# Kernel tuning notes

Hardware: AMD Instinct MI355X
Metric: run time of the kernel (lower is better)

Reference implementation:

```python
import jax, jax.numpy as jnp
import numpy as np

B, L, H = 64, 512, 512          # batch, max_len, hidden_size (code requires H == L)
ITEM = 50001                    # item_num + 1
TEMP = 0.2                      # gumbel-sigmoid temperature
EPS = 1e-20


def setup_inputs() -> dict:
    key = jax.random.key(0)
    ks = jax.random.split(key, 16)
    lin = lambda k: jax.random.normal(k, (L, L), jnp.float32) * (1.0 / np.sqrt(L))
    U = jax.random.uniform(ks[13], (L, H), jnp.float32)
    gumbel = -jnp.log(-jnp.log(U + EPS) + EPS)
    return {
        "positives": jax.random.randint(ks[0], (B, L), 0, ITEM),
        "mask": jax.random.randint(ks[1], (B, L), 0, 2).astype(jnp.int32),
        "item_emb": jax.random.normal(ks[2], (ITEM, H), jnp.float32) * 0.02,
        "pos_emb": jax.random.normal(ks[3], (L, H), jnp.float32) * 0.02,
        "Wz": lin(ks[4]),
        "Wv": lin(ks[5]),
        "Wq": lin(ks[6]),
        "Wk": lin(ks[7]),
        "gamma_q": jax.random.normal(ks[8], (L,), jnp.float32) * 0.02,
        "beta_q": jnp.zeros((L,), jnp.float32),
        "gamma_k": jax.random.normal(ks[9], (L,), jnp.float32) * 0.02,
        "beta_k": jnp.zeros((L,), jnp.float32),
        "sparse_w": jax.random.uniform(ks[10], (L, H), jnp.float32, 0.2, 0.8),
        "gumbel": gumbel,
    }


def reference(positives, mask, item_emb, pos_emb, Wz, Wv, Wq, Wk,
              gamma_q, beta_q, gamma_k, beta_k, sparse_w, gumbel):
    # ---- merge_attn_masks: True = masked ----
    pad = ~(mask.astype(bool))[:, None, :]                 # [B,1,L]
    future = jnp.triu(jnp.ones((L, L), bool), k=1)         # strictly upper
    merged = pad | future[None]                            # [B,L,L]
    attn_mask = (~jnp.eye(L, dtype=bool))[None] & merged   # keep diagonal unmasked

    # ---- embeddings ----
    x = item_emb[positives] + pos_emb[None]                # [B,L,H]

    # ---- GAU-style projections (Linear acts on last dim, y = x @ W^T) ----
    z = jax.nn.silu(x @ Wz.T)                              # [B,L,H]
    v = jax.nn.silu(x @ Wv.T)                              # [B,L,H]
    q = (z @ Wq.T) * gamma_q + beta_q                      # OffsetScale head 0
    k = (z @ Wk.T) * gamma_k + beta_k

    # ---- relu^2 attention with bool mask added then zeroed ----
    m = attn_mask.astype(q.dtype)
    a = jnp.einsum('bld,bmd->blm', q, k) + m               # torch adds bool as 0/1
    a = a * (1.0 - m)                                      # a * ~attn_mask

    # ---- gumbel-sigmoid sparse mask (broadcast [L,L] over batch) ----
    smask = jax.nn.sigmoid((jnp.log(sparse_w / (1.0 - sparse_w)) + gumbel) / TEMP)
    a = smask[None] * a

    a = jnp.square(jax.nn.relu(a)) / (L * H)
    return a @ v                                           # [B,L,H]
```

## Files before the change

kernel.cpp:

```cpp
#include <hip/hip_runtime.h>
#include <hip/hip_fp16.h>
#include <math.h>

typedef _Float16 f16;
typedef unsigned int u32;
typedef _Float16 f16x8 __attribute__((ext_vector_type(8)));
typedef _Float16 f16x4 __attribute__((ext_vector_type(4)));
typedef float    f32x4 __attribute__((ext_vector_type(4)));

constexpr int LEN  = 512;
constexpr int HID  = 512;
constexpr int BATCH = 64;

__device__ __forceinline__ void gload16(const f16* g, f16* l) {
    __builtin_amdgcn_global_load_lds((const __attribute__((address_space(1))) u32*)g,
                                     (__attribute__((address_space(3))) u32*)l,
                                     16, 0, 0);
}

__device__ __forceinline__ float silu_f(float v) {
    return v * __builtin_amdgcn_rcpf(1.f + __expf(-v));
}

#define TUNIT 12288
#define EPIP  136

__device__ __forceinline__ void stage_pass(const f16* __restrict__ g, f16* l) {
    const int tid = threadIdx.x;
    const int row = tid >> 2;
    const int sc  = (tid & 3) ^ ((row >> 1) & 3);
    gload16(g + (size_t)row * 512 + sc * 8, l + (tid >> 6) * 512);
}

__device__ __forceinline__ void stage_tile(const f16* __restrict__ A,
                                           const f16* __restrict__ B,
                                           int kt, f16* buf) {
    stage_pass(A + kt * 32,             buf);
    stage_pass(A + kt * 32 + 128 * 512, buf + 4096);
    stage_pass(B + kt * 32,             buf + 8192);
}

__device__ __forceinline__ void gemm8b(const f16* __restrict__ A,
                                       const f16* __restrict__ B,
                                       int ksteps, f16* lds, f32x4 acc[4][4])
{
    const int lane = threadIdx.x & 63;
    const int wv   = threadIdx.x >> 6;
    const int wr = wv >> 1, wc = wv & 1;
    const int mf = lane & 15;
    const int slot = ((lane >> 4) ^ ((mf >> 1) & 3)) * 8;
    const int aoff = (wr * 64 + mf) * 32 + slot;
    const int boff = (wc * 64 + mf) * 32 + slot + 8192;

    #pragma unroll
    for (int m = 0; m < 4; ++m)
        #pragma unroll
        for (int n = 0; n < 4; ++n)
            acc[m][n] = (f32x4){0.f, 0.f, 0.f, 0.f};

    stage_tile(A, B, 0, lds);
    stage_tile(A, B, 1, lds + TUNIT);
    asm volatile("s_waitcnt vmcnt(3)" ::: "memory");
    __builtin_amdgcn_s_barrier();

    int cb = 0;
    for (int kt = 0; kt < ksteps; ++kt) {
        f16* buf = lds + cb * TUNIT;
        f16x8 af[4], bf[4];
        #pragma unroll
        for (int m = 0; m < 4; ++m) af[m] = *(const f16x8*)(buf + aoff + m * 512);
        #pragma unroll
        for (int n = 0; n < 4; ++n) bf[n] = *(const f16x8*)(buf + boff + n * 512);
        if (kt + 2 < ksteps) {
            int nb = cb + 2; if (nb >= 3) nb -= 3;
            stage_tile(A, B, kt + 2, lds + nb * TUNIT);
        }
        asm volatile("s_waitcnt lgkmcnt(0)" ::: "memory");
        __builtin_amdgcn_sched_barrier(0);
        __builtin_amdgcn_s_setprio(1);
        #pragma unroll
        for (int m = 0; m < 4; ++m)
            #pragma unroll
            for (int n = 0; n < 4; ++n)
                acc[m][n] = __builtin_amdgcn_mfma_f32_16x16x32_f16(af[m], bf[n], acc[m][n], 0, 0, 0);
        __builtin_amdgcn_s_setprio(0);
        if (kt + 3 <= ksteps) {
            asm volatile("s_waitcnt vmcnt(3)" ::: "memory");
            __builtin_amdgcn_s_barrier();
        } else if (kt + 2 == ksteps) {
            asm volatile("s_waitcnt vmcnt(0)" ::: "memory");
            __builtin_amdgcn_s_barrier();
        }
        cb = cb + 1; if (cb >= 3) cb = 0;
    }
}

#define EPI_IDX() \
    const int lane = threadIdx.x & 63, wv_ = threadIdx.x >> 6;  \
    const int wr = wv_ >> 1, wc = wv_ & 1;                      \
    const int c0 = lane & 15, r0 = (lane >> 4) * 4;

__device__ __forceinline__ void copy_half(const f16* lds, f16* __restrict__ gout,
                                          int ldo, int h) {
    const int tid = threadIdx.x;
    #pragma unroll
    for (int ph = 0; ph < 4; ++ph) {
        const int r = ph * 32 + (tid >> 4);
        const int c = (tid & 15) * 8;
        *(f16x8*)(gout + (size_t)(h * 128 + r) * ldo + c) = *(const f16x8*)(lds + r * EPIP + c);
    }
}

__global__ __launch_bounds__(512, 4) void k_zv8(const f16* __restrict__ x,
                                                const f16* __restrict__ Wzh,
                                                const f16* __restrict__ Wvh,
                                                f16* __restrict__ z,
                                                f16* __restrict__ vt)
{
    __shared__ __align__(16) f16 lds[3 * TUNIT];
    const int bid = blockIdx.x;
    const int s  = (bid & 7) + 8 * (bid >> 6);
    const int ci = (bid >> 3) & 7;
    const f16* A; const f16* Bm; f16* gout;
    if (ci < 4) {
        A = x + (size_t)s * 256 * HID;
        Bm = Wzh + (size_t)ci * 128 * HID;
        gout = z + (size_t)s * 256 * HID + ci * 128;
    } else {
        const int ht = (ci - 4) >> 1, lh = (ci - 4) & 1;
        A = Wvh + (size_t)ht * 256 * HID;
        Bm = x + ((size_t)s * 256 + lh * 128) * HID;
        gout = vt + (size_t)(s >> 1) * LEN * HID + (size_t)ht * 256 * LEN
                  + (s & 1) * 256 + lh * 128;
    }
    f32x4 acc[4][4];
    gemm8b(A, Bm, HID / 32, lds, acc);
    __syncthreads();
    EPI_IDX();
    #pragma unroll
    for (int h = 0; h < 2; ++h) {
        if ((wr >> 1) == h) {
            const int rb = (wr & 1) * 64;
            #pragma unroll
            for (int m = 0; m < 4; ++m)
                #pragma unroll
                for (int n = 0; n < 4; ++n)
                    #pragma unroll
                    for (int i = 0; i < 4; ++i)
                        lds[(rb + m * 16 + r0 + i) * EPIP + wc * 64 + n * 16 + c0] =
                            (f16)silu_f(acc[m][n][i]);
        }
        __syncthreads();
        copy_half(lds, gout, 512, h);
        __syncthreads();
    }
}

__global__ __launch_bounds__(512, 4) void k_qkp8(const f16* __restrict__ z,
                                                 const f16* __restrict__ Wqh,
                                                 const f16* __restrict__ Wkh,
                                                 const float* __restrict__ gq,
                                                 const float* __restrict__ bq,
                                                 const float* __restrict__ gk,
                                                 const float* __restrict__ bk,
                                                 f16* __restrict__ qh,
                                                 f16* __restrict__ kh)
{
    __shared__ __align__(16) f16 lds[3 * TUNIT];
    const int bid = blockIdx.x;
    const int s  = (bid & 7) + 8 * (bid >> 6);
    const int ci = (bid >> 3) & 7;
    const bool isq = ci < 4;
    const int nt = ci & 3;
    const f16* W = isq ? Wqh : Wkh;
    const float* g  = isq ? gq : gk;
    const float* be = isq ? bq : bk;
    f16* outp = isq ? qh : kh;
    f32x4 acc[4][4];
    gemm8b(z + (size_t)s * 256 * HID, W + (size_t)nt * 128 * HID, HID / 32, lds, acc);
    __syncthreads();
    EPI_IDX();
    f16* gbase = outp + (size_t)s * 256 * HID + nt * 128;
    #pragma unroll
    for (int h = 0; h < 2; ++h) {
        if ((wr >> 1) == h) {
            const int rb = (wr & 1) * 64;
            #pragma unroll
            for (int n = 0; n < 4; ++n) {
                const int col = wc * 64 + n * 16 + c0;
                const int jg = nt * 128 + col;
                const float ga = g[jg], ba = be[jg];
                #pragma unroll
                for (int m = 0; m < 4; ++m)
                    #pragma unroll
                    for (int i = 0; i < 4; ++i)
                        lds[(rb + m * 16 + r0 + i) * EPIP + col] =
                            (f16)((acc[m][n][i] * ga + ba) * 1024.f);
            }
        }
        __syncthreads();
        copy_half(lds, gbase, 512, h);
        __syncthreads();
    }
}

__constant__ int LT6[6] = {0,0,1,1,1,1};
__constant__ int MT6[6] = {0,1,0,1,2,3};

__global__ __launch_bounds__(512, 4) void k_qk8(const f16* __restrict__ q,
                                                const f16* __restrict__ kmat,
                                                const int* __restrict__ mask,
                                                const float* __restrict__ smask,
                                                f16* __restrict__ p)
{
    __shared__ __align__(16) f16 lds[3 * TUNIT];
    const int bid = blockIdx.x;
    const int t = (bid >> 3) % 6;
    const int b = (bid & 7) + 8 * (bid / 48);
    const int lt = LT6[t], mt = MT6[t];
    const size_t boff = (size_t)b * LEN * HID;
    f32x4 acc[4][4];
    gemm8b(q + boff + (size_t)lt * 256 * HID,
           kmat + boff + (size_t)mt * 128 * HID, HID / 32, lds, acc);
    __syncthreads();
    EPI_IDX();
    f16* gbase = p + (size_t)b * LEN * LEN + (size_t)lt * 256 * LEN + mt * 128;
    #pragma unroll
    for (int h = 0; h < 2; ++h) {
        if ((wr >> 1) == h) {
            const int rb = (wr & 1) * 64;
            #pragma unroll
            for (int n = 0; n < 4; ++n) {
                const int col = wc * 64 + n * 16 + c0;
                const int m_g = mt * 128 + col;
                const int keepcol = mask[b * LEN + m_g];
                #pragma unroll
                for (int m = 0; m < 4; ++m)
                    #pragma unroll
                    for (int i = 0; i < 4; ++i) {
                        const int row = rb + m * 16 + r0 + i;
                        const int l_g = lt * 256 + h * 128 + row;
                        const bool keep = (l_g == m_g) || ((m_g <= l_g) && (keepcol != 0));
                        float v = keep ? acc[m][n][i] * smask[l_g * LEN + m_g] : 0.f;
                        v = fmaxf(v, 0.f);
                        lds[row * EPIP + col] = (f16)(v * v);
                    }
            }
        }
        __syncthreads();
        copy_half(lds, gbase, 512, h);
        __syncthreads();
    }
}

__global__ __launch_bounds__(512, 4) void k_pv8(const f16* __restrict__ p,
                                                const f16* __restrict__ vt,
                                                float* __restrict__ out)
{
    __shared__ __align__(16) f16 lds[3 * TUNIT];
    const int bid = blockIdx.x;
    const int inner = (bid >> 3) & 7;
    const int b = (bid & 7) + 8 * (bid >> 6);
    const int lt = 1 - (inner >> 2), ht = inner & 3;
    f32x4 acc[4][4];
    gemm8b(p + (size_t)b * LEN * LEN + (size_t)lt * 256 * LEN,
           vt + (size_t)b * HID * LEN + (size_t)ht * 128 * LEN,
           (lt + 1) * 8, lds, acc);
    EPI_IDX();
    const float SCALE = 3.4694469519536142e-18f;
    #pragma unroll
    for (int m = 0; m < 4; ++m)
        #pragma unroll
        for (int n = 0; n < 4; ++n) {
            const int h = ht * 128 + wc * 64 + n * 16 + c0;
            #pragma unroll
            for (int i = 0; i < 4; ++i) {
                const int l = lt * 256 + wr * 64 + m * 16 + r0 + i;
                out[(size_t)b * LEN * HID + (size_t)l * HID + h] = acc[m][n][i] * SCALE;
            }
        }
}

__global__ __launch_bounds__(256) void k_prep(const int* __restrict__ pos,
                                              const float* __restrict__ item_emb,
                                              const float* __restrict__ pos_emb,
                                              f16* __restrict__ x,
                                              const float* __restrict__ Wz,
                                              const float* __restrict__ Wv,
                                              const float* __restrict__ Wq,
                                              const float* __restrict__ Wk,
                                              f16* __restrict__ Wzh,
                                              f16* __restrict__ Wvh,
                                              f16* __restrict__ Wqh,
                                              f16* __restrict__ Wkh,
                                              const float* __restrict__ sw,
                                              const float* __restrict__ gum,
                                              float* __restrict__ smask)
{
    const int bid = blockIdx.x;
    const int tid = threadIdx.x;
    if (bid < 16384) {
        const int t = bid * 256 + tid;
        const int i = t >> 7;
        const int c = t & 127;
        const int l = i & (LEN - 1);
        const int item = pos[i];
        const float4 a  = ((const float4*)(item_emb + (size_t)item * HID))[c];
        const float4 b4 = ((const float4*)(pos_emb + (size_t)l * HID))[c];
        f16x4 o = { (f16)(a.x + b4.x), (f16)(a.y + b4.y),
                    (f16)(a.z + b4.z), (f16)(a.w + b4.w) };
        *(f16x4*)(x + (size_t)t * 4) = o;
    } else if (bid < 16384 + 1024) {
        const int r = bid - 16384;
        const int w = r >> 8;
        const float* s = (w == 0) ? Wz : (w == 1) ? Wv : (w == 2) ? Wq : Wk;
        f16* d = (w == 0) ? Wzh : (w == 1) ? Wvh : (w == 2) ? Wqh : Wkh;
        const int t = (r & 255) * 256 + tid;
        const float4 v = ((const float4*)s)[t];
        f16x4 o = { (f16)v.x, (f16)v.y, (f16)v.z, (f16)v.w };
        *(f16x4*)(d + (size_t)t * 4) = o;
    } else {
        const int t = (bid - 16384 - 1024) * 256 + tid;
        const float4 w4 = ((const float4*)sw)[t];
        const float4 g4 = ((const float4*)gum)[t];
        float4 o;
        o.x = __builtin_amdgcn_rcpf(1.f + __expf(-(__logf(w4.x / (1.f - w4.x)) + g4.x) * 5.f));
        o.y = __builtin_amdgcn_rcpf(1.f + __expf(-(__logf(w4.y / (1.f - w4.y)) + g4.y) * 5.f));
        o.z = __builtin_amdgcn_rcpf(1.f + __expf(-(__logf(w4.z / (1.f - w4.z)) + g4.z) * 5.f));
        o.w = __builtin_amdgcn_rcpf(1.f + __expf(-(__logf(w4.w / (1.f - w4.w)) + g4.w) * 5.f));
        ((float4*)smask)[t] = o;
    }
}

extern "C" void kernel_launch(void* const* d_in, const int* in_sizes, int n_in,
                              void* d_out, int out_size, void* d_ws, size_t ws_size,
                              hipStream_t stream)
{
    const int*   positives = (const int*)  d_in[0];
    const int*   mask      = (const int*)  d_in[1];
    const float* item_emb  = (const float*)d_in[2];
    const float* pos_emb   = (const float*)d_in[3];
    const float* Wz        = (const float*)d_in[4];
    const float* Wv        = (const float*)d_in[5];
    const float* Wq        = (const float*)d_in[6];
    const float* Wk        = (const float*)d_in[7];
    const float* gamma_q   = (const float*)d_in[8];
    const float* beta_q    = (const float*)d_in[9];
    const float* gamma_k   = (const float*)d_in[10];
    const float* beta_k    = (const float*)d_in[11];
    const float* sparse_w  = (const float*)d_in[12];
    const float* gumbel    = (const float*)d_in[13];
    float* out = (float*)d_out;

    char* ws = (char*)d_ws;
    const size_t BUFB = (size_t)BATCH * LEN * HID * sizeof(f16);
    f16* buf0 = (f16*)ws;
    f16* buf1 = (f16*)(ws + BUFB);
    f16* buf2 = (f16*)(ws + 2 * BUFB);
    f16* Wzh  = (f16*)(ws + 3 * BUFB);
    f16* Wvh  = Wzh + LEN * HID;
    f16* Wqh  = Wvh + LEN * HID;
    f16* Wkh  = Wqh + LEN * HID;
    float* smask = (float*)(Wkh + LEN * HID);
    f16* qh = (f16*)d_out;
    f16* kh = qh + (size_t)BATCH * LEN * HID;

    k_prep<<<16384 + 1024 + 256, 256, 0, stream>>>(
        positives, item_emb, pos_emb, buf0,
        Wz, Wv, Wq, Wk, Wzh, Wvh, Wqh, Wkh,
        sparse_w, gumbel, smask);

    k_zv8<<<1024, 512, 0, stream>>>(buf0, Wzh, Wvh, buf1, buf2);

    k_qkp8<<<1024, 512, 0, stream>>>(buf1, Wqh, Wkh,
                                     gamma_q, beta_q, gamma_k, beta_k, qh, kh);

    k_qk8<<<384, 512, 0, stream>>>(qh, kh, mask, smask, buf0);

    k_pv8<<<512, 512, 0, stream>>>(buf0, buf2, out);
}
```

Before: 344.1 us.

## Fuse QK score and PV kernels into single attention kernel

Replaces the separate QK-score kernel, which wrote masked relu^2 scores to a global buffer, and the PV GEMM kernel with one kernel. For each key tile it computes scores, applies the mask and sparse mask in registers, stages the f16 scores in LDS, and multiplies by V, accumulating the output without a global round trip. The cost is that each output tile recomputes the QK products for its row panel, once per hidden slice (4x redundant QK work). It also reads V fragments straight from global memory instead of staging them, and uses more LDS, cutting occupancy to 2 blocks. Q and K move from the output buffer into separate workspace buffers.

Result: slower. 672.8 us (+95.5%).

```diff
diff --git a/kernel.cpp b/kernel.cpp
--- a/kernel.cpp
+++ b/kernel.cpp
@@ -24,6 +24,7 @@
 
 #define TUNIT 12288
 #define EPIP  136
+#define SBUF  36864
 
 __device__ __forceinline__ void stage_pass(const f16* __restrict__ g, f16* l) {
     const int tid = threadIdx.x;
@@ -204,79 +205,92 @@
     }
 }
 
-__constant__ int LT6[6] = {0,0,1,1,1,1};
-__constant__ int MT6[6] = {0,1,0,1,2,3};
-
-__global__ __launch_bounds__(512, 4) void k_qk8(const f16* __restrict__ q,
-                                                const f16* __restrict__ kmat,
-                                                const int* __restrict__ mask,
-                                                const float* __restrict__ smask,
-                                                f16* __restrict__ p)
-{
-    __shared__ __align__(16) f16 lds[3 * TUNIT];
-    const int bid = blockIdx.x;
-    const int t = (bid >> 3) % 6;
-    const int b = (bid & 7) + 8 * (bid / 48);
-    const int lt = LT6[t], mt = MT6[t];
-    const size_t boff = (size_t)b * LEN * HID;
-    f32x4 acc[4][4];
-    gemm8b(q + boff + (size_t)lt * 256 * HID,
-           kmat + boff + (size_t)mt * 128 * HID, HID / 32, lds, acc);
-    __syncthreads();
-    EPI_IDX();
-    f16* gbase = p + (size_t)b * LEN * LEN + (size_t)lt * 256 * LEN + mt * 128;
-    #pragma unroll
-    for (int h = 0; h < 2; ++h) {
-        if ((wr >> 1) == h) {
-            const int rb = (wr & 1) * 64;
-            #pragma unroll
-            for (int n = 0; n < 4; ++n) {
-                const int col = wc * 64 + n * 16 + c0;
-                const int m_g = mt * 128 + col;
-                const int keepcol = mask[b * LEN + m_g];
-                #pragma unroll
-                for (int m = 0; m < 4; ++m)
-                    #pragma unroll
-                    for (int i = 0; i < 4; ++i) {
-                        const int row = rb + m * 16 + r0 + i;
-                        const int l_g = lt * 256 + h * 128 + row;
-                        const bool keep = (l_g == m_g) || ((m_g <= l_g) && (keepcol != 0));
-                        float v = keep ? acc[m][n][i] * smask[l_g * LEN + m_g] : 0.f;
-                        v = fmaxf(v, 0.f);
-                        lds[row * EPIP + col] = (f16)(v * v);
-                    }
-            }
-        }
-        __syncthreads();
-        copy_half(lds, gbase, 512, h);
-        __syncthreads();
-    }
-}
-
-__global__ __launch_bounds__(512, 4) void k_pv8(const f16* __restrict__ p,
-                                                const f16* __restrict__ vt,
-                                                float* __restrict__ out)
-{
-    __shared__ __align__(16) f16 lds[3 * TUNIT];
+__global__ __launch_bounds__(512, 2) void k_attn(const f16* __restrict__ q,
+                                                 const f16* __restrict__ kmat,
+                                                 const f16* __restrict__ vt,
+                                                 const int* __restrict__ mask,
+                                                 const float* __restrict__ smask,
+                                                 float* __restrict__ out)
+{
+    __shared__ __align__(16) f16 lds[SBUF + 32768];
     const int bid = blockIdx.x;
     const int inner = (bid >> 3) & 7;
     const int b = (bid & 7) + 8 * (bid >> 6);
-    const int lt = 1 - (inner >> 2), ht = inner & 3;
-    f32x4 acc[4][4];
-    gemm8b(p + (size_t)b * LEN * LEN + (size_t)lt * 256 * LEN,
-           vt + (size_t)b * HID * LEN + (size_t)ht * 128 * LEN,
-           (lt + 1) * 8, lds, acc);
-    EPI_IDX();
+    const int lt = 1 - (inner >> 2), hh = inner & 3;
+    const int nmt = (lt + 1) * 2;
+
+    const int lane = threadIdx.x & 63;
+    const int wv   = threadIdx.x >> 6;
+    const int wr = wv >> 1, wc = wv & 1;
+    const int c0 = lane & 15, r0 = (lane >> 4) * 4;
+    const int mf = lane & 15;
+    const int kfr = (lane >> 4) * 8;
+    const int slot = ((lane >> 4) ^ ((mf >> 1) & 3)) * 8;
+
+    const size_t boff = (size_t)b * LEN * HID;
+    const f16* qpan = q + boff + (size_t)lt * 256 * HID;
+    const f16* vrow = vt + (size_t)b * HID * LEN + (size_t)(hh * 128 + wc * 64 + mf) * LEN;
+
+    f32x4 acc_o[4][4];
+    #pragma unroll
+    for (int m = 0; m < 4; ++m)
+        #pragma unroll
+        for (int n = 0; n < 4; ++n)
+            acc_o[m][n] = (f32x4){0.f, 0.f, 0.f, 0.f};
+
+    for (int mt = 0; mt < nmt; ++mt) {
+        f32x4 acc_s[4][4];
+        gemm8b(qpan, kmat + boff + (size_t)mt * 128 * HID, HID / 32, lds, acc_s);
+
+        #pragma unroll
+        for (int n = 0; n < 4; ++n) {
+            const int c_l = wc * 64 + n * 16 + c0;
+            const int m_g = mt * 128 + c_l;
+            const int keepcol = mask[b * LEN + m_g];
+            const int sb = c_l >> 5;
+            const int col5 = c_l & 31;
+            #pragma unroll
+            for (int m = 0; m < 4; ++m)
+                #pragma unroll
+                for (int i = 0; i < 4; ++i) {
+                    const int r_l = wr * 64 + m * 16 + r0 + i;
+                    const int l_g = lt * 256 + r_l;
+                    const bool keep = (l_g == m_g) || ((m_g <= l_g) && (keepcol != 0));
+                    float v = keep ? acc_s[m][n][i] * smask[l_g * LEN + m_g] : 0.f;
+                    v = fmaxf(v, 0.f);
+                    const int sch = (col5 >> 3) ^ ((r_l >> 1) & 3);
+                    lds[SBUF + sb * 8192 + r_l * 32 + sch * 8 + (col5 & 7)] = (f16)(v * v);
+                }
+        }
+        __syncthreads();
+
+        #pragma unroll
+        for (int ks = 0; ks < 4; ++ks) {
+            f16x8 af[4], bf[4];
+            #pragma unroll
+            for (int m = 0; m < 4; ++m)
+                af[m] = *(const f16x8*)(lds + SBUF + ks * 8192 + (wr * 64 + mf) * 32 + slot + m * 512);
+            #pragma unroll
+            for (int n = 0; n < 4; ++n)
+                bf[n] = *(const f16x8*)(vrow + (size_t)n * 16 * LEN + mt * 128 + ks * 32 + kfr);
+            #pragma unroll
+            for (int m = 0; m < 4; ++m)
+                #pragma unroll
+                for (int n = 0; n < 4; ++n)
+                    acc_o[m][n] = __builtin_amdgcn_mfma_f32_16x16x32_f16(af[m], bf[n], acc_o[m][n], 0, 0, 0);
+        }
+    }
+
     const float SCALE = 3.4694469519536142e-18f;
     #pragma unroll
     for (int m = 0; m < 4; ++m)
         #pragma unroll
         for (int n = 0; n < 4; ++n) {
-            const int h = ht * 128 + wc * 64 + n * 16 + c0;
+            const int h_g = hh * 128 + wc * 64 + n * 16 + c0;
             #pragma unroll
             for (int i = 0; i < 4; ++i) {
-                const int l = lt * 256 + wr * 64 + m * 16 + r0 + i;
-                out[(size_t)b * LEN * HID + (size_t)l * HID + h] = acc[m][n][i] * SCALE;
+                const int l_g = lt * 256 + wr * 64 + m * 16 + r0 + i;
+                out[(size_t)b * LEN * HID + (size_t)l_g * HID + h_g] = acc_o[m][n][i] * SCALE;
             }
         }
 }
@@ -357,13 +371,13 @@
     f16* buf0 = (f16*)ws;
     f16* buf1 = (f16*)(ws + BUFB);
     f16* buf2 = (f16*)(ws + 2 * BUFB);
-    f16* Wzh  = (f16*)(ws + 3 * BUFB);
+    f16* qh   = (f16*)(ws + 3 * BUFB);
+    f16* kh   = (f16*)(ws + 4 * BUFB);
+    f16* Wzh  = (f16*)(ws + 5 * BUFB);
     f16* Wvh  = Wzh + LEN * HID;
     f16* Wqh  = Wvh + LEN * HID;
     f16* Wkh  = Wqh + LEN * HID;
     float* smask = (float*)(Wkh + LEN * HID);
-    f16* qh = (f16*)d_out;
-    f16* kh = qh + (size_t)BATCH * LEN * HID;
 
     k_prep<<<16384 + 1024 + 256, 256, 0, stream>>>(
         positives, item_emb, pos_emb, buf0,
@@ -375,7 +389,5 @@
     k_qkp8<<<1024, 512, 0, stream>>>(buf1, Wqh, Wkh,
                                      gamma_q, beta_q, gamma_k, beta_k, qh, kh);
 
-    k_qk8<<<384, 512, 0, stream>>>(qh, kh, mask, smask, buf0);
-
-    k_pv8<<<512, 512, 0, stream>>>(buf0, buf2, out);
-}
+    k_attn<<<512, 512, 0, stream>>>(qh, kh, buf2, mask, smask, out);
+}
```

## Enlarge GEMM tiles to 256x256 with four-stage split-staged LDS pipeline

Applied to the files above, without the earlier changes.

Every GEMM kernel now computes a 256x256 output tile per block instead of 256x128. Each wave holds an 8x4 accumulator array, and each k-step is split into two MFMA halves, with the A and B loads for three steps ahead staged between them. This raises arithmetic intensity and reuse of staged LDS data and halves the grid sizes. The cost is more LDS (four 32KB stages) and more registers, so occupancy drops to 2 blocks per CU. The small grids, especially 192 blocks for QK^T, may underfill the GPU's CUs. q/k buffers also move from the output buffer to the workspace.

Measured after the change: 392.2 us. 14.0% more time.

```diff
diff --git a/kernel.cpp b/kernel.cpp
--- a/kernel.cpp
+++ b/kernel.cpp
@@ -22,8 +22,8 @@
     return v * __builtin_amdgcn_rcpf(1.f + __expf(-v));
 }
 
-#define TUNIT 12288
-#define EPIP  136
+#define TP 16384
+#define EP 264
 
 __device__ __forceinline__ void stage_pass(const f16* __restrict__ g, f16* l) {
     const int tid = threadIdx.x;
@@ -34,47 +34,52 @@
 
 __device__ __forceinline__ void stage_tile(const f16* __restrict__ A,
                                            const f16* __restrict__ B,
-                                           int kt, f16* buf) {
-    stage_pass(A + kt * 32,             buf);
-    stage_pass(A + kt * 32 + 128 * 512, buf + 4096);
-    stage_pass(B + kt * 32,             buf + 8192);
-}
-
-__device__ __forceinline__ void gemm8b(const f16* __restrict__ A,
+                                           int t, f16* buf) {
+    stage_pass(A + t * 32,             buf);
+    stage_pass(A + t * 32 + 128 * 512, buf + 4096);
+    stage_pass(B + t * 32,             buf + 8192);
+    stage_pass(B + t * 32 + 128 * 512, buf + 12288);
+}
+
+__device__ __forceinline__ void gemm8p(const f16* __restrict__ A,
                                        const f16* __restrict__ B,
-                                       int ksteps, f16* lds, f32x4 acc[4][4])
+                                       int nt, f16* lds, f32x4 acc[8][4])
 {
     const int lane = threadIdx.x & 63;
     const int wv   = threadIdx.x >> 6;
-    const int wr = wv >> 1, wc = wv & 1;
+    const int wr = wv >> 2, wc = wv & 3;
     const int mf = lane & 15;
     const int slot = ((lane >> 4) ^ ((mf >> 1) & 3)) * 8;
-    const int aoff = (wr * 64 + mf) * 32 + slot;
-    const int boff = (wc * 64 + mf) * 32 + slot + 8192;
-
-    #pragma unroll
-    for (int m = 0; m < 4; ++m)
+    const int abase = wr * 4096 + mf * 32 + slot;
+    const int bbase = 8192 + (wc >> 1) * 4096 + ((wc & 1) * 64 + mf) * 32 + slot;
+
+    #pragma unroll
+    for (int m = 0; m < 8; ++m)
         #pragma unroll
         for (int n = 0; n < 4; ++n)
             acc[m][n] = (f32x4){0.f, 0.f, 0.f, 0.f};
 
     stage_tile(A, B, 0, lds);
-    stage_tile(A, B, 1, lds + TUNIT);
-    asm volatile("s_waitcnt vmcnt(3)" ::: "memory");
+    stage_tile(A, B, 1, lds + TP);
+    stage_tile(A, B, 2, lds + 2 * TP);
+    asm volatile("s_waitcnt vmcnt(8)" ::: "memory");
     __builtin_amdgcn_s_barrier();
 
-    int cb = 0;
-    for (int kt = 0; kt < ksteps; ++kt) {
-        f16* buf = lds + cb * TUNIT;
+    for (int t = 0; t < nt; ++t) {
+        f16* buf  = lds + (t & 3) * TP;
+        f16* nbuf = lds + ((t + 3) & 3) * TP;
+        const bool st = (t + 3 < nt);
         f16x8 af[4], bf[4];
-        #pragma unroll
-        for (int m = 0; m < 4; ++m) af[m] = *(const f16x8*)(buf + aoff + m * 512);
-        #pragma unroll
-        for (int n = 0; n < 4; ++n) bf[n] = *(const f16x8*)(buf + boff + n * 512);
-        if (kt + 2 < ksteps) {
-            int nb = cb + 2; if (nb >= 3) nb -= 3;
-            stage_tile(A, B, kt + 2, lds + nb * TUNIT);
-        }
+
+        #pragma unroll
+        for (int m = 0; m < 4; ++m) af[m] = *(const f16x8*)(buf + abase + m * 512);
+        #pragma unroll
+        for (int n = 0; n < 4; ++n) bf[n] = *(const f16x8*)(buf + bbase + n * 512);
+        if (st) {
+            stage_pass(A + (t + 3) * 32,             nbuf);
+            stage_pass(A + (t + 3) * 32 + 128 * 512, nbuf + 4096);
+        }
+        __builtin_amdgcn_s_barrier();
         asm volatile("s_waitcnt lgkmcnt(0)" ::: "memory");
         __builtin_amdgcn_sched_barrier(0);
         __builtin_amdgcn_s_setprio(1);
@@ -84,70 +89,82 @@
             for (int n = 0; n < 4; ++n)
                 acc[m][n] = __builtin_amdgcn_mfma_f32_16x16x32_f16(af[m], bf[n], acc[m][n], 0, 0, 0);
         __builtin_amdgcn_s_setprio(0);
-        if (kt + 3 <= ksteps) {
-            asm volatile("s_waitcnt vmcnt(3)" ::: "memory");
-            __builtin_amdgcn_s_barrier();
-        } else if (kt + 2 == ksteps) {
-            asm volatile("s_waitcnt vmcnt(0)" ::: "memory");
-            __builtin_amdgcn_s_barrier();
-        }
-        cb = cb + 1; if (cb >= 3) cb = 0;
+        __builtin_amdgcn_s_barrier();
+
+        #pragma unroll
+        for (int m = 0; m < 4; ++m) af[m] = *(const f16x8*)(buf + abase + (m + 4) * 512);
+        if (st) {
+            stage_pass(B + (t + 3) * 32,             nbuf + 8192);
+            stage_pass(B + (t + 3) * 32 + 128 * 512, nbuf + 12288);
+        }
+        __builtin_amdgcn_s_barrier();
+        asm volatile("s_waitcnt lgkmcnt(0)" ::: "memory");
+        __builtin_amdgcn_sched_barrier(0);
+        __builtin_amdgcn_s_setprio(1);
+        #pragma unroll
+        for (int m = 0; m < 4; ++m)
+            #pragma unroll
+            for (int n = 0; n < 4; ++n)
+                acc[m + 4][n] = __builtin_amdgcn_mfma_f32_16x16x32_f16(af[m], bf[n], acc[m + 4][n], 0, 0, 0);
+        __builtin_amdgcn_s_setprio(0);
+        if (t < nt - 3)       { asm volatile("s_waitcnt vmcnt(8)" ::: "memory"); }
+        else if (t == nt - 3) { asm volatile("s_waitcnt vmcnt(4)" ::: "memory"); }
+        else if (t == nt - 2) { asm volatile("s_waitcnt vmcnt(0)" ::: "memory"); }
+        __builtin_amdgcn_s_barrier();
     }
 }
 
 #define EPI_IDX() \
     const int lane = threadIdx.x & 63, wv_ = threadIdx.x >> 6;  \
-    const int wr = wv_ >> 1, wc = wv_ & 1;                      \
+    const int wr = wv_ >> 2, wc = wv_ & 3;                      \
     const int c0 = lane & 15, r0 = (lane >> 4) * 4;
 
 __device__ __forceinline__ void copy_half(const f16* lds, f16* __restrict__ gout,
                                           int ldo, int h) {
     const int tid = threadIdx.x;
     #pragma unroll
-    for (int ph = 0; ph < 4; ++ph) {
-        const int r = ph * 32 + (tid >> 4);
-        const int c = (tid & 15) * 8;
-        *(f16x8*)(gout + (size_t)(h * 128 + r) * ldo + c) = *(const f16x8*)(lds + r * EPIP + c);
-    }
-}
-
-__global__ __launch_bounds__(512, 4) void k_zv8(const f16* __restrict__ x,
+    for (int ph = 0; ph < 8; ++ph) {
+        const int r = ph * 16 + (tid >> 5);
+        const int c = (tid & 31) * 8;
+        *(f16x8*)(gout + (size_t)(h * 128 + r) * ldo + c) = *(const f16x8*)(lds + r * EP + c);
+    }
+}
+
+__global__ __launch_bounds__(512, 2) void k_zv8(const f16* __restrict__ x,
                                                 const f16* __restrict__ Wzh,
                                                 const f16* __restrict__ Wvh,
                                                 f16* __restrict__ z,
                                                 f16* __restrict__ vt)
 {
-    __shared__ __align__(16) f16 lds[3 * TUNIT];
-    const int bid = blockIdx.x;
-    const int s  = (bid & 7) + 8 * (bid >> 6);
-    const int ci = (bid >> 3) & 7;
+    __shared__ __align__(16) f16 lds[4 * TP];
+    const int bid = blockIdx.x;
+    const int s  = (bid & 7) + 8 * (bid >> 5);
+    const int ci = (bid >> 3) & 3;
     const f16* A; const f16* Bm; f16* gout;
-    if (ci < 4) {
+    if (ci < 2) {
         A = x + (size_t)s * 256 * HID;
-        Bm = Wzh + (size_t)ci * 128 * HID;
-        gout = z + (size_t)s * 256 * HID + ci * 128;
+        Bm = Wzh + (size_t)ci * 256 * HID;
+        gout = z + (size_t)s * 256 * HID + ci * 256;
     } else {
-        const int ht = (ci - 4) >> 1, lh = (ci - 4) & 1;
+        const int ht = ci - 2;
         A = Wvh + (size_t)ht * 256 * HID;
-        Bm = x + ((size_t)s * 256 + lh * 128) * HID;
-        gout = vt + (size_t)(s >> 1) * LEN * HID + (size_t)ht * 256 * LEN
-                  + (s & 1) * 256 + lh * 128;
-    }
-    f32x4 acc[4][4];
-    gemm8b(A, Bm, HID / 32, lds, acc);
+        Bm = x + (size_t)s * 256 * HID;
+        gout = vt + (size_t)(s >> 1) * LEN * HID + (size_t)ht * 256 * LEN + (s & 1) * 256;
+    }
+    f32x4 acc[8][4];
+    gemm8p(A, Bm, 16, lds, acc);
+    EPI_IDX();
     __syncthreads();
-    EPI_IDX();
     #pragma unroll
     for (int h = 0; h < 2; ++h) {
-        if ((wr >> 1) == h) {
-            const int rb = (wr & 1) * 64;
-            #pragma unroll
-            for (int m = 0; m < 4; ++m)
+        if (wr == h) {
+            #pragma unroll
+            for (int m = 0; m < 8; ++m)
                 #pragma unroll
                 for (int n = 0; n < 4; ++n)
                     #pragma unroll
                     for (int i = 0; i < 4; ++i)
-                        lds[(rb + m * 16 + r0 + i) * EPIP + wc * 64 + n * 16 + c0] =
+                        lds[(m * 16 + r0 + i) * EP + wc * 64 + n * 16 + c0] =
                             (f16)silu_f(acc[m][n][i]);
         }
         __syncthreads();
@@ -156,7 +173,7 @@
     }
 }
 
-__global__ __launch_bounds__(512, 4) void k_qkp8(const f16* __restrict__ z,
+__global__ __launch_bounds__(512, 2) void k_qkp8(const f16* __restrict__ z,
                                                  const f16* __restrict__ Wqh,
                                                  const f16* __restrict__ Wkh,
                                                  const float* __restrict__ gq,
@@ -166,35 +183,34 @@
                                                  f16* __restrict__ qh,
                                                  f16* __restrict__ kh)
 {
-    __shared__ __align__(16) f16 lds[3 * TUNIT];
-    const int bid = blockIdx.x;
-    const int s  = (bid & 7) + 8 * (bid >> 6);
-    const int ci = (bid >> 3) & 7;
-    const bool isq = ci < 4;
-    const int nt = ci & 3;
+    __shared__ __align__(16) f16 lds[4 * TP];
+    const int bid = blockIdx.x;
+    const int s  = (bid & 7) + 8 * (bid >> 5);
+    const int ci = (bid >> 3) & 3;
+    const bool isq = ci < 2;
+    const int ct = ci & 1;
     const f16* W = isq ? Wqh : Wkh;
     const float* g  = isq ? gq : gk;
     const float* be = isq ? bq : bk;
     f16* outp = isq ? qh : kh;
-    f32x4 acc[4][4];
-    gemm8b(z + (size_t)s * 256 * HID, W + (size_t)nt * 128 * HID, HID / 32, lds, acc);
+    f32x4 acc[8][4];
+    gemm8p(z + (size_t)s * 256 * HID, W + (size_t)ct * 256 * HID, 16, lds, acc);
+    EPI_IDX();
+    f16* gbase = outp + (size_t)s * 256 * HID + ct * 256;
     __syncthreads();
-    EPI_IDX();
-    f16* gbase = outp + (size_t)s * 256 * HID + nt * 128;
     #pragma unroll
     for (int h = 0; h < 2; ++h) {
-        if ((wr >> 1) == h) {
-            const int rb = (wr & 1) * 64;
+        if (wr == h) {
             #pragma unroll
             for (int n = 0; n < 4; ++n) {
                 const int col = wc * 64 + n * 16 + c0;
-                const int jg = nt * 128 + col;
+                const int jg = ct * 256 + col;
                 const float ga = g[jg], ba = be[jg];
                 #pragma unroll
-                for (int m = 0; m < 4; ++m)
+                for (int m = 0; m < 8; ++m)
                     #pragma unroll
                     for (int i = 0; i < 4; ++i)
-                        lds[(rb + m * 16 + r0 + i) * EPIP + col] =
+                        lds[(m * 16 + r0 + i) * EP + col] =
                             (f16)((acc[m][n][i] * ga + ba) * 1024.f);
             }
         }
@@ -204,46 +220,45 @@
     }
 }
 
-__constant__ int LT6[6] = {0,0,1,1,1,1};
-__constant__ int MT6[6] = {0,1,0,1,2,3};
-
-__global__ __launch_bounds__(512, 4) void k_qk8(const f16* __restrict__ q,
+__constant__ int LT3[3] = {0, 1, 1};
+__constant__ int MT3[3] = {0, 0, 1};
+
+__global__ __launch_bounds__(512, 2) void k_qk8(const f16* __restrict__ q,
                                                 const f16* __restrict__ kmat,
                                                 const int* __restrict__ mask,
                                                 const float* __restrict__ smask,
                                                 f16* __restrict__ p)
 {
-    __shared__ __align__(16) f16 lds[3 * TUNIT];
-    const int bid = blockIdx.x;
-    const int t = (bid >> 3) % 6;
-    const int b = (bid & 7) + 8 * (bid / 48);
-    const int lt = LT6[t], mt = MT6[t];
+    __shared__ __align__(16) f16 lds[4 * TP];
+    const int bid = blockIdx.x;
+    const int tt = (bid >> 3) % 3;
+    const int b = (bid & 7) + 8 * (bid / 24);
+    const int lt = LT3[tt], mt = MT3[tt];
     const size_t boff = (size_t)b * LEN * HID;
-    f32x4 acc[4][4];
-    gemm8b(q + boff + (size_t)lt * 256 * HID,
-           kmat + boff + (size_t)mt * 128 * HID, HID / 32, lds, acc);
+    f32x4 acc[8][4];
+    gemm8p(q + boff + (size_t)lt * 256 * HID,
+           kmat + boff + (size_t)mt * 256 * HID, 16, lds, acc);
+    EPI_IDX();
+    f16* gbase = p + (size_t)b * LEN * LEN + (size_t)lt * 256 * LEN + mt * 256;
     __syncthreads();
-    EPI_IDX();
-    f16* gbase = p + (size_t)b * LEN * LEN + (size_t)lt * 256 * LEN + mt * 128;
     #pragma unroll
     for (int h = 0; h < 2; ++h) {
-        if ((wr >> 1) == h) {
-            const int rb = (wr & 1) * 64;
+        if (wr == h) {
             #pragma unroll
             for (int n = 0; n < 4; ++n) {
                 const int col = wc * 64 + n * 16 + c0;
-                const int m_g = mt * 128 + col;
+                const int m_g = mt * 256 + col;
                 const int keepcol = mask[b * LEN + m_g];
                 #pragma unroll
-                for (int m = 0; m < 4; ++m)
+                for (int m = 0; m < 8; ++m)
                     #pragma unroll
                     for (int i = 0; i < 4; ++i) {
-                        const int row = rb + m * 16 + r0 + i;
+                        const int row = m * 16 + r0 + i;
                         const int l_g = lt * 256 + h * 128 + row;
                         const bool keep = (l_g == m_g) || ((m_g <= l_g) && (keepcol != 0));
                         float v = keep ? acc[m][n][i] * smask[l_g * LEN + m_g] : 0.f;
                         v = fmaxf(v, 0.f);
-                        lds[row * EPIP + col] = (f16)(v * v);
+                        lds[row * EP + col] = (f16)(v * v);
                     }
             }
         }
@@ -253,30 +268,30 @@
     }
 }
 
-__global__ __launch_bounds__(512, 4) void k_pv8(const f16* __restrict__ p,
+__global__ __launch_bounds__(512, 2) void k_pv8(const f16* __restrict__ p,
                                                 const f16* __restrict__ vt,
                                                 float* __restrict__ out)
 {
-    __shared__ __align__(16) f16 lds[3 * TUNIT];
-    const int bid = blockIdx.x;
-    const int inner = (bid >> 3) & 7;
-    const int b = (bid & 7) + 8 * (bid >> 6);
-    const int lt = 1 - (inner >> 2), ht = inner & 3;
-    f32x4 acc[4][4];
-    gemm8b(p + (size_t)b * LEN * LEN + (size_t)lt * 256 * LEN,
-           vt + (size_t)b * HID * LEN + (size_t)ht * 128 * LEN,
+    __shared__ __align__(16) f16 lds[4 * TP];
+    const int bid = blockIdx.x;
+    const int inner = (bid >> 3) & 3;
+    const int b = (bid & 7) + 8 * (bid >> 5);
+    const int lt = 1 - (inner >> 1), ht = inner & 1;
+    f32x4 acc[8][4];
+    gemm8p(p + (size_t)b * LEN * LEN + (size_t)lt * 256 * LEN,
+           vt + (size_t)b * HID * LEN + (size_t)ht * 256 * LEN,
            (lt + 1) * 8, lds, acc);
     EPI_IDX();
     const float SCALE = 3.4694469519536142e-18f;
     #pragma unroll
-    for (int m = 0; m < 4; ++m)
+    for (int m = 0; m < 8; ++m)
         #pragma unroll
         for (int n = 0; n < 4; ++n) {
-            const int h = ht * 128 + wc * 64 + n * 16 + c0;
+            const int h_g = ht * 256 + wc * 64 + n * 16 + c0;
             #pragma unroll
             for (int i = 0; i < 4; ++i) {
-                const int l = lt * 256 + wr * 64 + m * 16 + r0 + i;
-                out[(size_t)b * LEN * HID + (size_t)l * HID + h] = acc[m][n][i] * SCALE;
+                const int l_g = lt * 256 + wr * 128 + m * 16 + r0 + i;
+                out[(size_t)b * LEN * HID + (size_t)l_g * HID + h_g] = acc[m][n][i] * SCALE;
             }
         }
 }
@@ -357,25 +372,25 @@
     f16* buf0 = (f16*)ws;
     f16* buf1 = (f16*)(ws + BUFB);
     f16* buf2 = (f16*)(ws + 2 * BUFB);
-    f16* Wzh  = (f16*)(ws + 3 * BUFB);
+    f16* qh   = (f16*)(ws + 3 * BUFB);
+    f16* kh   = (f16*)(ws + 4 * BUFB);
+    f16* Wzh  = (f16*)(ws + 5 * BUFB);
     f16* Wvh  = Wzh + LEN * HID;
     f16* Wqh  = Wvh + LEN * HID;
     f16* Wkh  = Wqh + LEN * HID;
     float* smask = (float*)(Wkh + LEN * HID);
-    f16* qh = (f16*)d_out;
-    f16* kh = qh + (size_t)BATCH * LEN * HID;
 
     k_prep<<<16384 + 1024 + 256, 256, 0, stream>>>(
         positives, item_emb, pos_emb, buf0,
         Wz, Wv, Wq, Wk, Wzh, Wvh, Wqh, Wkh,
         sparse_w, gumbel, smask);
 
-    k_zv8<<<1024, 512, 0, stream>>>(buf0, Wzh, Wvh, buf1, buf2);
-
-    k_qkp8<<<1024, 512, 0, stream>>>(buf1, Wqh, Wkh,
-                                     gamma_q, beta_q, gamma_k, beta_k, qh, kh);
-
-    k_qk8<<<384, 512, 0, stream>>>(qh, kh, mask, smask, buf0);
-
-    k_pv8<<<512, 512, 0, stream>>>(buf0, buf2, out);
-}
+    k_zv8<<<512, 512, 0, stream>>>(buf0, Wzh, Wvh, buf1, buf2);
+
+    k_qkp8<<<512, 512, 0, stream>>>(buf1, Wqh, Wkh,
+                                    gamma_q, beta_q, gamma_k, beta_k, qh, kh);
+
+    k_qk8<<<192, 512, 0, stream>>>(qh, kh, mask, smask, buf0);
+
+    k_pv8<<<256, 512, 0, stream>>>(buf0, buf2, out);
+}
```
